# Performance work log

Measured on AMD Instinct MI355X. Metric: run time of the kernel, lower is better.

The kernel has to match this reference:

```python
import jax, jax.numpy as jnp
import numpy as np

# Repo globals / config
VOCAB_SIZE = 14
TOK_DIM = 8
POS_DIM = 8
D_MODEL = TOK_DIM + POS_DIM  # 16
MAX_SEQ_LEN = 2048
N_HEADS = 2
HEAD_DIM = 3
ATTN_DIM = N_HEADS * HEAD_DIM  # 6
FFN_DIM = 3
B, T = 16, 2048
EPS = 1e-5


def _ln(x, w, b):
    m = jnp.mean(x, axis=-1, keepdims=True)
    v = jnp.var(x, axis=-1, keepdims=True)
    return (x - m) * jax.lax.rsqrt(v + EPS) * w + b


def setup_inputs() -> dict:
    key = jax.random.key(0)
    ks = jax.random.split(key, 20)
    g = lambda k, shape: (jax.random.normal(k, shape, jnp.float32) * 0.1)
    return {
        "idx": jax.random.randint(ks[0], (B, T), 0, VOCAB_SIZE),
        "tok_emb": g(ks[1], (VOCAB_SIZE, TOK_DIM)),
        "pos_enc": g(ks[2], (MAX_SEQ_LEN, POS_DIM)),
        "Wq": g(ks[3], (ATTN_DIM, POS_DIM)),
        "Wk": g(ks[4], (ATTN_DIM, POS_DIM)),
        "Wv": g(ks[5], (ATTN_DIM, TOK_DIM)),
        "Wo": g(ks[6], (D_MODEL, ATTN_DIM)),
        "ln1_w": jnp.ones((D_MODEL,), jnp.float32),
        "ln1_b": jnp.zeros((D_MODEL,), jnp.float32),
        "ln2_w": jnp.ones((D_MODEL,), jnp.float32),
        "ln2_b": jnp.zeros((D_MODEL,), jnp.float32),
        "lnf_w": jnp.ones((D_MODEL,), jnp.float32),
        "lnf_b": jnp.zeros((D_MODEL,), jnp.float32),
        "W1": g(ks[7], (FFN_DIM, D_MODEL)),
        "b1": jnp.zeros((FFN_DIM,), jnp.float32),
        "W2": g(ks[8], (D_MODEL, FFN_DIM)),
        "b2": jnp.zeros((D_MODEL,), jnp.float32),
        "Wh": g(ks[9], (TOK_DIM, D_MODEL)),
    }


def reference(idx, tok_emb, pos_enc, Wq, Wk, Wv, Wo,
              ln1_w, ln1_b, ln2_w, ln2_b, lnf_w, lnf_b,
              W1, b1, W2, b2, Wh):
    Bq, Tq = idx.shape
    tok = tok_emb[idx]                                  # [B,T,TOK_DIM]
    pos = jnp.broadcast_to(pos_enc[:Tq][None], (Bq, Tq, POS_DIM))
    x = jnp.concatenate([tok, pos], axis=-1)            # [B,T,D_MODEL]
    h = _ln(x, ln1_w, ln1_b)
    x_tok = h[..., :TOK_DIM]
    x_pos = h[..., TOK_DIM:]
    # projections (torch Linear: y = x @ W.T)
    q = (x_pos @ Wq.T).reshape(Bq, Tq, N_HEADS, HEAD_DIM).transpose(0, 2, 1, 3)
    k = (x_pos @ Wk.T).reshape(Bq, Tq, N_HEADS, HEAD_DIM).transpose(0, 2, 1, 3)
    v = (x_tok @ Wv.T).reshape(Bq, Tq, N_HEADS, HEAD_DIM).transpose(0, 2, 1, 3)
    scores = jnp.einsum('bhqd,bhkd->bhqk', q, k) / jnp.sqrt(jnp.float32(HEAD_DIM))
    mask = jnp.tril(jnp.ones((Tq, Tq), dtype=bool))
    scores = jnp.where(mask[None, None], scores, -jnp.inf)
    attn = jax.nn.softmax(scores, axis=-1)
    out = jnp.einsum('bhqk,bhkd->bhqd', attn, v)
    out = out.transpose(0, 2, 1, 3).reshape(Bq, Tq, ATTN_DIM)
    x = x + out @ Wo.T
    h2 = _ln(x, ln2_w, ln2_b)
    x = x + (jax.nn.gelu(h2 @ W1.T + b1, approximate=False) @ W2.T + b2)
    x = _ln(x, lnf_w, lnf_b)
    return (x @ Wh.T) @ tok_emb.T                       # tied head -> [B,T,VOCAB]
```

## Files before the change

### kernel.cpp

```cpp
#include <hip/hip_runtime.h>
#include <math.h>

#define BB    16
#define TT    2048
#define VOCAB 14
#define TOKD  8
#define POSD  8
#define DM    16
#define NH    2
#define HD    3
#define AD    6
#define FFND  3

#define NTOK  (BB*TT)
#define BH    (BB*NH)
#define TPB   36
#define NTILE (BH*TPB)

struct P {
    const int*   idx;
    const float* tok_emb;
    const float* pos_enc;
    const float* Wq;
    const float* Wk;
    const float* Wv;
    const float* Wo;
    const float* ln1w;
    const float* ln1b;
    const float* ln2w;
    const float* ln2b;
    const float* lnfw;
    const float* lnfb;
    const float* W1;
    const float* b1;
    const float* W2;
    const float* b2;
    const float* Wh;
    float*       out;
    float4*      pbuf;
};

__device__ __forceinline__ void ln1_of(const P& p, int b, int t, float* h) {
    float x[DM];
    int tok = p.idx[b * TT + t];
    #pragma unroll
    for (int j = 0; j < TOKD; ++j) x[j]        = p.tok_emb[tok * TOKD + j];
    #pragma unroll
    for (int j = 0; j < POSD; ++j) x[TOKD + j] = p.pos_enc[t * POSD + j];

    float m = 0.f;
    #pragma unroll
    for (int j = 0; j < DM; ++j) m += x[j];
    m *= (1.f / DM);
    float v = 0.f;
    #pragma unroll
    for (int j = 0; j < DM; ++j) { float d = x[j] - m; v += d * d; }
    v *= (1.f / DM);
    float rs = rsqrtf(v + 1e-5f);
    #pragma unroll
    for (int j = 0; j < DM; ++j)
        h[j] = (x[j] - m) * rs * p.ln1w[j] + p.ln1b[j];
}

#define LOADKV(it)                                                             \
    float4 Kr = skv[((kw + (it)) << 1)];                                       \
    float4 Vr = skv[((kw + (it)) << 1) + 1];                                   \
    float k0 = Kr.x, k1 = Kr.y, k2 = Kr.z;                                     \
    float v0 = Vr.x, v1 = Vr.y, v2 = Vr.z;

__global__ __launch_bounds__(256, 5) void attn_kernel(P p) {
    __shared__ float4 skv[512];
    __shared__ float4 sq[256];
    __shared__ float4 spart[1024];

    const int tid  = threadIdx.x;
    int tile = blockIdx.x;
    int bh   = tile / TPB;
    int r    = tile - bh * TPB;
    int s    = 0;
    while (((s + 1) * (s + 2)) / 2 <= r) ++s;
    int c    = r - (s * (s + 1)) / 2;
    int b    = bh >> 1;
    int hh   = bh & 1;

    {
        float hK[DM];
        ln1_of(p, b, (c << 8) + tid, hK);
        float k0=0.f,k1=0.f,k2=0.f,v0=0.f,v1=0.f,v2=0.f;
        const float* wk  = p.Wk + (hh * 3) * 8;
        const float* wv_ = p.Wv + (hh * 3) * 8;
        #pragma unroll
        for (int j = 0; j < 8; ++j) {
            k0 = fmaf(wk[j],      hK[TOKD + j], k0);
            k1 = fmaf(wk[8 + j],  hK[TOKD + j], k1);
            k2 = fmaf(wk[16 + j], hK[TOKD + j], k2);
            v0 = fmaf(wv_[j],      hK[j], v0);
            v1 = fmaf(wv_[8 + j],  hK[j], v1);
            v2 = fmaf(wv_[16 + j], hK[j], v2);
        }
        skv[(tid << 1)]     = make_float4(k0, k1, k2, 0.f);
        skv[(tid << 1) + 1] = make_float4(v0, v1, v2, 0.f);

        float hQ[DM];
        if (c != s) {
            ln1_of(p, b, (s << 8) + tid, hQ);
        } else {
            #pragma unroll
            for (int j = 0; j < DM; ++j) hQ[j] = hK[j];
        }
        const float QS = 1.4426950408889634f / 1.7320508075688772f;
        float q0=0.f,q1=0.f,q2=0.f;
        const float* wq = p.Wq + (hh * 3) * 8;
        #pragma unroll
        for (int j = 0; j < 8; ++j) {
            q0 = fmaf(wq[j],      hQ[TOKD + j], q0);
            q1 = fmaf(wq[8 + j],  hQ[TOKD + j], q1);
            q2 = fmaf(wq[16 + j], hQ[TOKD + j], q2);
        }
        sq[tid] = make_float4(q0 * QS, q1 * QS, q2 * QS, 0.f);
    }
    __syncthreads();

    int wv   = tid >> 6;
    int lane = tid & 63;
    int kw   = wv << 6;

    float4 qr[4];
    #pragma unroll
    for (int j = 0; j < 4; ++j) qr[j] = sq[(j << 6) + lane];

    float ac[4][4];
    #pragma unroll
    for (int j = 0; j < 4; ++j)
        ac[j][0] = ac[j][1] = ac[j][2] = ac[j][3] = 0.f;

    if (c < s) {
        #pragma unroll 8
        for (int it = 0; it < 64; ++it) {
            LOADKV(it)
            #pragma unroll
            for (int j = 0; j < 4; ++j) {
                float sc = fmaf(qr[j].x, k0, fmaf(qr[j].y, k1, qr[j].z * k2));
                float pr = __builtin_amdgcn_exp2f(sc);
                ac[j][0] = fmaf(pr, v0, ac[j][0]);
                ac[j][1] = fmaf(pr, v1, ac[j][1]);
                ac[j][2] = fmaf(pr, v2, ac[j][2]);
                ac[j][3] += pr;
            }
        }
    } else {
        #pragma unroll
        for (int j = 0; j < 4; ++j) {
            if (j < wv) continue;
            if (j == wv) {
                #pragma unroll 4
                for (int it = 0; it < 64; ++it) {
                    LOADKV(it)
                    float sc = fmaf(qr[j].x, k0, fmaf(qr[j].y, k1, qr[j].z * k2));
                    float pr = __builtin_amdgcn_exp2f(sc);
                    pr = (it <= lane) ? pr : 0.f;
                    ac[j][0] = fmaf(pr, v0, ac[j][0]);
                    ac[j][1] = fmaf(pr, v1, ac[j][1]);
                    ac[j][2] = fmaf(pr, v2, ac[j][2]);
                    ac[j][3] += pr;
                }
            } else {
                #pragma unroll 4
                for (int it = 0; it < 64; ++it) {
                    LOADKV(it)
                    float sc = fmaf(qr[j].x, k0, fmaf(qr[j].y, k1, qr[j].z * k2));
                    float pr = __builtin_amdgcn_exp2f(sc);
                    ac[j][0] = fmaf(pr, v0, ac[j][0]);
                    ac[j][1] = fmaf(pr, v1, ac[j][1]);
                    ac[j][2] = fmaf(pr, v2, ac[j][2]);
                    ac[j][3] += pr;
                }
            }
        }
    }

    #pragma unroll
    for (int j = 0; j < 4; ++j)
        spart[(wv << 8) + (j << 6) + lane] =
            make_float4(ac[j][0], ac[j][1], ac[j][2], ac[j][3]);
    __syncthreads();

    float4 p0 = spart[tid];
    float4 p1 = spart[256 + tid];
    float4 p2 = spart[512 + tid];
    float4 p3 = spart[768 + tid];
    float4 acc = make_float4(p0.x+p1.x+p2.x+p3.x, p0.y+p1.y+p2.y+p3.y,
                             p0.z+p1.z+p2.z+p3.z, p0.w+p1.w+p2.w+p3.w);
    p.pbuf[((size_t)bh * 8 + c) * TT + (s << 8) + tid] = acc;
}

__global__ __launch_bounds__(256) void epi_kernel(P p) {
    int gid = blockIdx.x * 256 + threadIdx.x;
    if (gid >= NTOK) return;
    int t = gid & (TT - 1);
    int b = gid >> 11;
    int s = t >> 8;

    float x[DM];
    int tok = p.idx[gid];
    #pragma unroll
    for (int j = 0; j < TOKD; ++j) x[j]        = p.tok_emb[tok * TOKD + j];
    #pragma unroll
    for (int j = 0; j < POSD; ++j) x[TOKD + j] = p.pos_enc[t * POSD + j];

    float att[AD];
    #pragma unroll
    for (int hh = 0; hh < NH; ++hh) {
        const float4* pp = p.pbuf + ((size_t)(b * NH + hh) * 8) * TT + t;
        float4 acc = pp[0];
        for (int c = 1; c <= s; ++c) {
            float4 e = pp[(size_t)c * TT];
            acc.x += e.x; acc.y += e.y; acc.z += e.z; acc.w += e.w;
        }
        float inv = 1.f / acc.w;
        att[hh*3+0] = acc.x * inv;
        att[hh*3+1] = acc.y * inv;
        att[hh*3+2] = acc.z * inv;
    }

    float xo[DM];
    #pragma unroll
    for (int j = 0; j < DM; ++j) {
        float sacc = x[j];
        #pragma unroll
        for (int a = 0; a < AD; ++a) sacc = fmaf(p.Wo[j * AD + a], att[a], sacc);
        xo[j] = sacc;
    }

    float m = 0.f;
    #pragma unroll
    for (int j = 0; j < DM; ++j) m += xo[j];
    m *= (1.f / DM);
    float v = 0.f;
    #pragma unroll
    for (int j = 0; j < DM; ++j) { float d = xo[j] - m; v += d * d; }
    v *= (1.f / DM);
    float rs = rsqrtf(v + 1e-5f);
    float h2[DM];
    #pragma unroll
    for (int j = 0; j < DM; ++j)
        h2[j] = (xo[j] - m) * rs * p.ln2w[j] + p.ln2b[j];

    float g[FFND];
    #pragma unroll
    for (int cc = 0; cc < FFND; ++cc) {
        float f = p.b1[cc];
        #pragma unroll
        for (int j = 0; j < DM; ++j) f = fmaf(p.W1[cc * DM + j], h2[j], f);
        g[cc] = 0.5f * f * (1.f + erff(f * 0.70710678118654752f));
    }
    float x2[DM];
    #pragma unroll
    for (int j = 0; j < DM; ++j) {
        float sacc = xo[j] + p.b2[j];
        #pragma unroll
        for (int cc = 0; cc < FFND; ++cc) sacc = fmaf(p.W2[j * FFND + cc], g[cc], sacc);
        x2[j] = sacc;
    }

    m = 0.f;
    #pragma unroll
    for (int j = 0; j < DM; ++j) m += x2[j];
    m *= (1.f / DM);
    v = 0.f;
    #pragma unroll
    for (int j = 0; j < DM; ++j) { float d = x2[j] - m; v += d * d; }
    v *= (1.f / DM);
    rs = rsqrtf(v + 1e-5f);
    float y[DM];
    #pragma unroll
    for (int j = 0; j < DM; ++j)
        y[j] = (x2[j] - m) * rs * p.lnfw[j] + p.lnfb[j];

    float t8[TOKD];
    #pragma unroll
    for (int pp = 0; pp < TOKD; ++pp) {
        float sacc = 0.f;
        #pragma unroll
        for (int j = 0; j < DM; ++j) sacc = fmaf(p.Wh[pp * DM + j], y[j], sacc);
        t8[pp] = sacc;
    }
    float* op = p.out + (size_t)gid * VOCAB;
    #pragma unroll
    for (int vcb = 0; vcb < VOCAB; ++vcb) {
        float sacc = 0.f;
        #pragma unroll
        for (int pp = 0; pp < TOKD; ++pp)
            sacc = fmaf(t8[pp], p.tok_emb[vcb * TOKD + pp], sacc);
        op[vcb] = sacc;
    }
}

extern "C" void kernel_launch(void* const* d_in, const int* in_sizes, int n_in,
                              void* d_out, int out_size, void* d_ws, size_t ws_size,
                              hipStream_t stream) {
    P p;
    p.idx     = (const int*)d_in[0];
    p.tok_emb = (const float*)d_in[1];
    p.pos_enc = (const float*)d_in[2];
    p.Wq      = (const float*)d_in[3];
    p.Wk      = (const float*)d_in[4];
    p.Wv      = (const float*)d_in[5];
    p.Wo      = (const float*)d_in[6];
    p.ln1w    = (const float*)d_in[7];
    p.ln1b    = (const float*)d_in[8];
    p.ln2w    = (const float*)d_in[9];
    p.ln2b    = (const float*)d_in[10];
    p.lnfw    = (const float*)d_in[11];
    p.lnfb    = (const float*)d_in[12];
    p.W1      = (const float*)d_in[13];
    p.b1      = (const float*)d_in[14];
    p.W2      = (const float*)d_in[15];
    p.b2      = (const float*)d_in[16];
    p.Wh      = (const float*)d_in[17];
    p.out     = (float*)d_out;
    p.pbuf    = (float4*)d_ws;

    attn_kernel<<<NTILE, 256, 0, stream>>>(p);
    epi_kernel<<<NTOK / 256, 256, 0, stream>>>(p);
}
```

Measured before the change: 126.5 us.

## Split attention key tiles to 128 keys and alias shared memory for occupancy

Key chunks shrink from 256 to 128 tokens while query tiles stay at 256. This gives 2304 blocks per launch with a finer triangular schedule, and fully masked query-subtile and key-chunk pairs are skipped. Shared memory is aliased (spart reuses the skv/sq space behind an extra barrier) and launch bounds rise to 8 blocks per SM to raise occupancy. The epilogue now reduces up to 16 partial buffers per token instead of 8, which adds workspace traffic, and the extra K/V LN recomputation costs more per key.

```diff
diff --git a/kernel.cpp b/kernel.cpp
--- a/kernel.cpp
+++ b/kernel.cpp
@@ -14,8 +14,8 @@
 
 #define NTOK  (BB*TT)
 #define BH    (BB*NH)
-#define TPB   36
-#define NTILE (BH*TPB)
+#define NMAIN 2048
+#define NTILE3 2304
 
 struct P {
     const int*   idx;
@@ -68,46 +68,34 @@
     float k0 = Kr.x, k1 = Kr.y, k2 = Kr.z;                                     \
     float v0 = Vr.x, v1 = Vr.y, v2 = Vr.z;
 
-__global__ __launch_bounds__(256, 5) void attn_kernel(P p) {
-    __shared__ float4 skv[512];
-    __shared__ float4 sq[256];
-    __shared__ float4 spart[1024];
-
-    const int tid  = threadIdx.x;
-    int tile = blockIdx.x;
-    int bh   = tile / TPB;
-    int r    = tile - bh * TPB;
-    int s    = 0;
-    while (((s + 1) * (s + 2)) / 2 <= r) ++s;
-    int c    = r - (s * (s + 1)) / 2;
-    int b    = bh >> 1;
-    int hh   = bh & 1;
+__global__ __launch_bounds__(256, 8) void attn_kernel(P p) {
+    __shared__ float4 smem[1024];
+    float4* skv = smem;
+    float4* sq  = smem + 256;
+    float4* spart = smem;
+
+    const int tid = threadIdx.x;
+    int bid = blockIdx.x;
+    int bh, s, c;
+    if (bid < NMAIN) {
+        bh = bid >> 6;
+        int rr = bid & 63;
+        s = 0;
+        while ((s + 1) * (s + 1) <= rr) ++s;
+        c = rr - s * s;
+    } else {
+        int k = bid - NMAIN;
+        bh = k >> 3;
+        s  = k & 7;
+        c  = 2 * s + 1;
+    }
+    int b  = bh >> 1;
+    int hh = bh & 1;
+    int ko = (c << 7) - (s << 8);
 
     {
-        float hK[DM];
-        ln1_of(p, b, (c << 8) + tid, hK);
-        float k0=0.f,k1=0.f,k2=0.f,v0=0.f,v1=0.f,v2=0.f;
-        const float* wk  = p.Wk + (hh * 3) * 8;
-        const float* wv_ = p.Wv + (hh * 3) * 8;
-        #pragma unroll
-        for (int j = 0; j < 8; ++j) {
-            k0 = fmaf(wk[j],      hK[TOKD + j], k0);
-            k1 = fmaf(wk[8 + j],  hK[TOKD + j], k1);
-            k2 = fmaf(wk[16 + j], hK[TOKD + j], k2);
-            v0 = fmaf(wv_[j],      hK[j], v0);
-            v1 = fmaf(wv_[8 + j],  hK[j], v1);
-            v2 = fmaf(wv_[16 + j], hK[j], v2);
-        }
-        skv[(tid << 1)]     = make_float4(k0, k1, k2, 0.f);
-        skv[(tid << 1) + 1] = make_float4(v0, v1, v2, 0.f);
-
         float hQ[DM];
-        if (c != s) {
-            ln1_of(p, b, (s << 8) + tid, hQ);
-        } else {
-            #pragma unroll
-            for (int j = 0; j < DM; ++j) hQ[j] = hK[j];
-        }
+        ln1_of(p, b, (s << 8) + tid, hQ);
         const float QS = 1.4426950408889634f / 1.7320508075688772f;
         float q0=0.f,q1=0.f,q2=0.f;
         const float* wq = p.Wq + (hh * 3) * 8;
@@ -118,12 +106,36 @@
             q2 = fmaf(wq[16 + j], hQ[TOKD + j], q2);
         }
         sq[tid] = make_float4(q0 * QS, q1 * QS, q2 * QS, 0.f);
+
+        if (tid < 128) {
+            float hK[DM];
+            if (ko == 0) {
+                #pragma unroll
+                for (int j = 0; j < DM; ++j) hK[j] = hQ[j];
+            } else {
+                ln1_of(p, b, (c << 7) + tid, hK);
+            }
+            float k0=0.f,k1=0.f,k2=0.f,v0=0.f,v1=0.f,v2=0.f;
+            const float* wk  = p.Wk + (hh * 3) * 8;
+            const float* wv_ = p.Wv + (hh * 3) * 8;
+            #pragma unroll
+            for (int j = 0; j < 8; ++j) {
+                k0 = fmaf(wk[j],      hK[TOKD + j], k0);
+                k1 = fmaf(wk[8 + j],  hK[TOKD + j], k1);
+                k2 = fmaf(wk[16 + j], hK[TOKD + j], k2);
+                v0 = fmaf(wv_[j],      hK[j], v0);
+                v1 = fmaf(wv_[8 + j],  hK[j], v1);
+                v2 = fmaf(wv_[16 + j], hK[j], v2);
+            }
+            skv[(tid << 1)]     = make_float4(k0, k1, k2, 0.f);
+            skv[(tid << 1) + 1] = make_float4(v0, v1, v2, 0.f);
+        }
     }
     __syncthreads();
 
     int wv   = tid >> 6;
     int lane = tid & 63;
-    int kw   = wv << 6;
+    int kw   = wv << 5;
 
     float4 qr[4];
     #pragma unroll
@@ -134,9 +146,9 @@
     for (int j = 0; j < 4; ++j)
         ac[j][0] = ac[j][1] = ac[j][2] = ac[j][3] = 0.f;
 
-    if (c < s) {
+    if (ko < 0) {
         #pragma unroll 8
-        for (int it = 0; it < 64; ++it) {
+        for (int it = 0; it < 32; ++it) {
             LOADKV(it)
             #pragma unroll
             for (int j = 0; j < 4; ++j) {
@@ -149,24 +161,14 @@
             }
         }
     } else {
+        int klo = ko + kw;
         #pragma unroll
         for (int j = 0; j < 4; ++j) {
-            if (j < wv) continue;
-            if (j == wv) {
-                #pragma unroll 4
-                for (int it = 0; it < 64; ++it) {
-                    LOADKV(it)
-                    float sc = fmaf(qr[j].x, k0, fmaf(qr[j].y, k1, qr[j].z * k2));
-                    float pr = __builtin_amdgcn_exp2f(sc);
-                    pr = (it <= lane) ? pr : 0.f;
-                    ac[j][0] = fmaf(pr, v0, ac[j][0]);
-                    ac[j][1] = fmaf(pr, v1, ac[j][1]);
-                    ac[j][2] = fmaf(pr, v2, ac[j][2]);
-                    ac[j][3] += pr;
-                }
-            } else {
-                #pragma unroll 4
-                for (int it = 0; it < 64; ++it) {
+            int qlo = j << 6;
+            if (klo > qlo + 63) continue;
+            if (klo + 31 <= qlo) {
+                #pragma unroll 8
+                for (int it = 0; it < 32; ++it) {
                     LOADKV(it)
                     float sc = fmaf(qr[j].x, k0, fmaf(qr[j].y, k1, qr[j].z * k2));
                     float pr = __builtin_amdgcn_exp2f(sc);
@@ -175,9 +177,23 @@
                     ac[j][2] = fmaf(pr, v2, ac[j][2]);
                     ac[j][3] += pr;
                 }
+            } else {
+                #pragma unroll 8
+                for (int it = 0; it < 32; ++it) {
+                    LOADKV(it)
+                    float sc = fmaf(qr[j].x, k0, fmaf(qr[j].y, k1, qr[j].z * k2));
+                    float pr = __builtin_amdgcn_exp2f(sc);
+                    pr = (klo + it <= qlo + lane) ? pr : 0.f;
+                    ac[j][0] = fmaf(pr, v0, ac[j][0]);
+                    ac[j][1] = fmaf(pr, v1, ac[j][1]);
+                    ac[j][2] = fmaf(pr, v2, ac[j][2]);
+                    ac[j][3] += pr;
+                }
             }
         }
     }
+
+    __syncthreads();
 
     #pragma unroll
     for (int j = 0; j < 4; ++j)
@@ -191,7 +207,7 @@
     float4 p3 = spart[768 + tid];
     float4 acc = make_float4(p0.x+p1.x+p2.x+p3.x, p0.y+p1.y+p2.y+p3.y,
                              p0.z+p1.z+p2.z+p3.z, p0.w+p1.w+p2.w+p3.w);
-    p.pbuf[((size_t)bh * 8 + c) * TT + (s << 8) + tid] = acc;
+    p.pbuf[((size_t)(bh << 4) + c) * TT + (s << 8) + tid] = acc;
 }
 
 __global__ __launch_bounds__(256) void epi_kernel(P p) {
@@ -199,7 +215,7 @@
     if (gid >= NTOK) return;
     int t = gid & (TT - 1);
     int b = gid >> 11;
-    int s = t >> 8;
+    int s16 = t >> 7;
 
     float x[DM];
     int tok = p.idx[gid];
@@ -211,9 +227,9 @@
     float att[AD];
     #pragma unroll
     for (int hh = 0; hh < NH; ++hh) {
-        const float4* pp = p.pbuf + ((size_t)(b * NH + hh) * 8) * TT + t;
+        const float4* pp = p.pbuf + ((size_t)((b * NH + hh) << 4)) * TT + t;
         float4 acc = pp[0];
-        for (int c = 1; c <= s; ++c) {
+        for (int c = 1; c <= s16; ++c) {
             float4 e = pp[(size_t)c * TT];
             acc.x += e.x; acc.y += e.y; acc.z += e.z; acc.w += e.w;
         }
@@ -321,6 +337,6 @@
     p.out     = (float*)d_out;
     p.pbuf    = (float4*)d_ws;
 
-    attn_kernel<<<NTILE, 256, 0, stream>>>(p);
+    attn_kernel<<<NTILE3, 256, 0, stream>>>(p);
     epi_kernel<<<NTOK / 256, 256, 0, stream>>>(p);
 }
```

Result: slower. 138.3 us (+9.4%).
